# Performance work log

Measured on AMD Instinct MI355X. Metric: run time of the kernel, lower is better.

Reference implementation:

```python
import jax, jax.numpy as jnp
import numpy as np

N = 50000   # num nodes
E = 800000  # num edges
D = 128     # embedding dim
EPS = 1e-5


def setup_inputs() -> dict:
    key = jax.random.key(0)
    ks = jax.random.split(key, 16)
    x = jnp.arange(N, dtype=jnp.int32)
    edge_index = jax.random.randint(ks[0], (2, E), 0, N, dtype=jnp.int32)
    weight = jax.random.uniform(ks[1], (E,), dtype=jnp.float32)
    emb = jax.random.normal(ks[2], (N, D), dtype=jnp.float32)
    # layer dims: 128->128, 128->64, 64->32
    dims = [(128, 128), (128, 64), (64, 32)]
    inp = {"x": x, "edge_index": edge_index, "weight": weight, "emb": emb}
    for i, (fi, fo) in enumerate(dims, start=1):
        s = 1.0 / np.sqrt(fi)
        inp[f"W{i}"] = jax.random.uniform(ks[3 * i], (fi, fo), dtype=jnp.float32, minval=-s, maxval=s)
        inp[f"b{i}"] = jnp.zeros((fo,), dtype=jnp.float32)
        inp[f"g{i}"] = jnp.ones((fo,), dtype=jnp.float32)
        inp[f"be{i}"] = jnp.zeros((fo,), dtype=jnp.float32)
    return inp


def _gcn_conv(h, src, dst, w, W, b):
    # PyG GCNConv: linear, add self-loops (weight 1), symmetric normalization, scatter-add
    h = h @ W  # [N, Fout]
    loop = jnp.arange(N, dtype=src.dtype)
    src_l = jnp.concatenate([src, loop])
    dst_l = jnp.concatenate([dst, loop])
    w_l = jnp.concatenate([w, jnp.ones((N,), w.dtype)])
    deg = jax.ops.segment_sum(w_l, dst_l, num_segments=N)
    dinv = jnp.where(deg > 0, jax.lax.rsqrt(jnp.maximum(deg, 1e-30)), 0.0)
    norm = dinv[src_l] * w_l * dinv[dst_l]  # [E+N]
    msg = h[src_l] * norm[:, None]          # gather + scale, [E+N, Fout]
    out = jax.ops.segment_sum(msg, dst_l, num_segments=N)
    return out + b


def _batch_norm(h, g, be):
    mu = h.mean(axis=0)
    var = h.var(axis=0)  # biased, as torch BN uses for normalization
    return (h - mu) * jax.lax.rsqrt(var + EPS) * g + be


def reference(x, edge_index, weight, emb,
              W1, b1, g1, be1,
              W2, b2, g2, be2,
              W3, b3, g3, be3):
    src, dst = edge_index[0], edge_index[1]
    h = emb[x]  # embedding lookup
    h = _batch_norm(_gcn_conv(h, src, dst, weight, W1, b1), g1, be1)
    h = jax.nn.relu(h)
    h = _batch_norm(_gcn_conv(h, src, dst, weight, W2, b2), g2, be2)
    h = jax.nn.relu(h)
    h = _batch_norm(_gcn_conv(h, src, dst, weight, W3, b3), g3, be3)
    return h
```

## Files before the change

### kernel.cpp

```cpp
#include <hip/hip_runtime.h>
#include <hip/hip_bf16.h>

#define BN_EPS 1e-5f
#define FIXSCALE 16777216.0f
#define FIXINV   5.9604644775390625e-08
#define LOWMASK  0xFFFFFFFFFFULL

typedef __attribute__((ext_vector_type(8))) short bf16x8;
typedef __attribute__((ext_vector_type(4))) float f32x4;

__device__ __forceinline__ unsigned short bfu(float v) {
  return __bfloat16_as_ushort(__float2bfloat16(v));
}
__device__ __forceinline__ unsigned int pk_bf2(float a, float b) {
  return (unsigned int)bfu(a) | ((unsigned int)bfu(b) << 16);
}
__device__ __forceinline__ float bf_lo(unsigned int u) { return __uint_as_float(u << 16); }
__device__ __forceinline__ float bf_hi(unsigned int u) { return __uint_as_float(u & 0xFFFF0000u); }

__device__ __forceinline__ void fma8(float* a, uint4 u, float c) {
  a[0] += bf_lo(u.x) * c; a[1] += bf_hi(u.x) * c;
  a[2] += bf_lo(u.y) * c; a[3] += bf_hi(u.y) * c;
  a[4] += bf_lo(u.z) * c; a[5] += bf_hi(u.z) * c;
  a[6] += bf_lo(u.w) * c; a[7] += bf_hi(u.w) * c;
}

__device__ __forceinline__ float4 load4(const float* p) { return *(const float4*)p; }
__device__ __forceinline__ float4 load4(const unsigned short* p) {
  uint2 u = *(const uint2*)p;
  return make_float4(bf_lo(u.x), bf_hi(u.x), bf_lo(u.y), bf_hi(u.y));
}

template <int FIN, int FOUT>
constexpr int gemm_lds_bytes() {
  int stage = (64 * (FIN + 8) + FOUT * (FIN + 8)) * 2;
  int cb = 64 * (FOUT + 4) * 4;
  return stage > cb ? stage : cb;
}


__global__ void prep_k(const float* __restrict__ W1, const float* __restrict__ W2,
                       const float* __restrict__ W3, unsigned short* __restrict__ wt1,
                       unsigned short* __restrict__ wt2, unsigned short* __restrict__ wt3,
                       unsigned long long* __restrict__ packed, int n) {
  int idx = blockIdx.x * 256 + threadIdx.x;
  if (idx < n) packed[idx] = 0ULL;
  if (idx < 128 * 128) {
    int c = idx >> 7, k = idx & 127;
    wt1[idx] = bfu(W1[k * 128 + c]);
  } else if (idx < 128 * 128 + 128 * 64) {
    int i2 = idx - 128 * 128;
    int c = i2 >> 7, k = i2 & 127;
    wt2[i2] = bfu(W2[k * 64 + c]);
  } else if (idx < 128 * 128 + 128 * 64 + 64 * 32) {
    int i2 = idx - 128 * 128 - 128 * 64;
    int c = i2 >> 6, k = i2 & 63;
    wt3[i2] = bfu(W3[k * 32 + c]);
  }
}


__global__ __launch_bounds__(256) void hist_gemm1_k(
    const float* __restrict__ emb, const int* __restrict__ x,
    const unsigned short* __restrict__ wt1, unsigned short* __restrict__ outA,
    const int* __restrict__ dst, const float* __restrict__ w,
    unsigned long long* __restrict__ packed, int* __restrict__ rank,
    int n, int e, int gx) {
  constexpr int FIN = 128, FOUT = 128;
  constexpr int C4 = FIN / 4;
  constexpr int ldH = FIN + 8;
  constexpr int ldC = FOUT + 4;
  constexpr int NCT = FOUT / 16;
  constexpr int NK = FIN / 32;
  __shared__ __align__(16) char smem[64 * ldH * 2];
  unsigned short* Ht = (unsigned short*)smem;
  float* Cs = (float*)smem;

  if ((int)blockIdx.x >= gx) {
    int i = ((blockIdx.x - gx) * 256 + threadIdx.x) * 2;
    if (i + 1 < e) {
      int2 d2 = *(const int2*)(dst + i);
      float2 w2 = *(const float2*)(w + i);
      unsigned long long a0 = (1ULL << 40) | (unsigned long long)__float2uint_rn(w2.x * FIXSCALE);
      unsigned long long a1 = (1ULL << 40) | (unsigned long long)__float2uint_rn(w2.y * FIXSCALE);
      unsigned long long o0 = atomicAdd(&packed[d2.x], a0);
      unsigned long long o1 = atomicAdd(&packed[d2.y], a1);
      *(int2*)(rank + i) = make_int2((int)(o0 >> 40), (int)(o1 >> 40));
    } else if (i < e) {
      unsigned long long fw = (unsigned long long)__float2uint_rn(w[i] * FIXSCALE);
      unsigned long long old = atomicAdd(&packed[dst[i]], (1ULL << 40) | fw);
      rank[i] = (int)(old >> 40);
    }
    return;
  }

  const int t = threadIdx.x;
  const int r0 = blockIdx.x * 64;

  constexpr int NH = 64 * C4 / 256;
#pragma unroll
  for (int i = 0; i < NH; ++i) {
    int idx = t + 256 * i;
    int r = idx / C4, c4 = idx % C4;
    int gr = r0 + r;
    if (gr < n) {
      int srow = x[gr];
      float4 v = *(const float4*)(emb + (size_t)srow * FIN + c4 * 4);
      ushort4 p;
      p.x = bfu(v.x); p.y = bfu(v.y); p.z = bfu(v.z); p.w = bfu(v.w);
      *(ushort4*)&Ht[r * ldH + c4 * 4] = p;
    }
  }
  __syncthreads();

  const int wv = t >> 6;
  const int l = t & 63;
  const int l15 = l & 15;
  const int kg = l >> 4;
  const int arow = wv * 16 + l15;

  f32x4 acc[NCT];
#pragma unroll
  for (int c = 0; c < NCT; ++c) acc[c] = (f32x4){0.f, 0.f, 0.f, 0.f};

#pragma unroll
  for (int kk = 0; kk < NK; ++kk) {
    bf16x8 a = *(const bf16x8*)&Ht[arow * ldH + kk * 32 + kg * 8];
#pragma unroll
    for (int c = 0; c < NCT; ++c) {
      bf16x8 b = *(const bf16x8*)&wt1[(size_t)(c * 16 + l15) * FIN + kk * 32 + kg * 8];
      acc[c] = __builtin_amdgcn_mfma_f32_16x16x32_bf16(a, b, acc[c], 0, 0, 0);
    }
  }
  __syncthreads();

#pragma unroll
  for (int ph = 0; ph < 2; ++ph) {
    if ((wv >> 1) == ph) {
#pragma unroll
      for (int c = 0; c < NCT; ++c)
#pragma unroll
        for (int m = 0; m < 4; ++m)
          Cs[((wv & 1) * 16 + kg * 4 + m) * ldC + c * 16 + l15] = acc[c][m];
    }
    __syncthreads();
#pragma unroll
    for (int i = 0; i < 2; ++i) {
      int u = t + 256 * i;
      int r = u / (FOUT / 8), c8 = u % (FOUT / 8);
      int gr = r0 + ph * 32 + r;
      if (gr < n) {
        const float* p = &Cs[r * ldC + c8 * 8];
        float4 v0 = *(const float4*)p;
        float4 v1 = *(const float4*)(p + 4);
        uint4 o;
        o.x = pk_bf2(v0.x, v0.y); o.y = pk_bf2(v0.z, v0.w);
        o.z = pk_bf2(v1.x, v1.y); o.w = pk_bf2(v1.z, v1.w);
        *(uint4*)&outA[(size_t)gr * FOUT + c8 * 8] = o;
      }
    }
    if (ph == 0) __syncthreads();
  }
}


template <typename TIN, int FIN, int FOUT, bool BNIN>
__global__ __launch_bounds__(256) void gemm_mfma_k(
    const TIN* __restrict__ H, const float* __restrict__ scale, const float* __restrict__ shift,
    const unsigned short* __restrict__ WtG, unsigned short* __restrict__ out, int n) {
  constexpr int C4 = FIN / 4;
  constexpr int ldH = FIN + 8;
  constexpr int ldW = FIN + 8;
  constexpr int ldC = FOUT + 4;
  constexpr int NCT = FOUT / 16;
  constexpr int NK = FIN / 32;
  constexpr int HT_SH = 64 * ldH;

  __shared__ __align__(16) char smem[gemm_lds_bytes<FIN, FOUT>()];
  unsigned short* Ht = (unsigned short*)smem;
  unsigned short* Wt = (unsigned short*)smem + HT_SH;
  float* Cs = (float*)smem;

  const int t = threadIdx.x;
  const int r0 = blockIdx.x * 64;

  constexpr int NH = 64 * C4 / 256;
#pragma unroll
  for (int i = 0; i < NH; ++i) {
    int idx = t + 256 * i;
    int r = idx / C4, c4 = idx % C4;
    int gr = r0 + r;
    if (gr < n) {
      float4 v = load4(H + (size_t)gr * FIN + c4 * 4);
      if (BNIN) {
        float4 sc = *(const float4*)(scale + c4 * 4);
        float4 sh = *(const float4*)(shift + c4 * 4);
        v.x = fmaxf(v.x * sc.x + sh.x, 0.f);
        v.y = fmaxf(v.y * sc.y + sh.y, 0.f);
        v.z = fmaxf(v.z * sc.z + sh.z, 0.f);
        v.w = fmaxf(v.w * sc.w + sh.w, 0.f);
      }
      ushort4 p;
      p.x = bfu(v.x); p.y = bfu(v.y); p.z = bfu(v.z); p.w = bfu(v.w);
      *(ushort4*)&Ht[r * ldH + c4 * 4] = p;
    }
  }
  constexpr int NWU = FOUT * FIN / 8 / 256;
#pragma unroll
  for (int i = 0; i < NWU; ++i) {
    int idx = t + 256 * i;
    int wr = idx / (FIN / 8), w8 = idx % (FIN / 8);
    *(uint4*)&Wt[wr * ldW + w8 * 8] = *(const uint4*)&WtG[wr * FIN + w8 * 8];
  }
  __syncthreads();

  const int w = t >> 6;
  const int l = t & 63;
  const int l15 = l & 15;
  const int kg = l >> 4;
  const int arow = w * 16 + l15;

  f32x4 acc[NCT];
#pragma unroll
  for (int c = 0; c < NCT; ++c) acc[c] = (f32x4){0.f, 0.f, 0.f, 0.f};

#pragma unroll
  for (int kk = 0; kk < NK; ++kk) {
    bf16x8 a = *(const bf16x8*)&Ht[arow * ldH + kk * 32 + kg * 8];
#pragma unroll
    for (int c = 0; c < NCT; ++c) {
      bf16x8 b = *(const bf16x8*)&Wt[(c * 16 + l15) * ldW + kk * 32 + kg * 8];
      acc[c] = __builtin_amdgcn_mfma_f32_16x16x32_bf16(a, b, acc[c], 0, 0, 0);
    }
  }
  __syncthreads();

#pragma unroll
  for (int c = 0; c < NCT; ++c)
#pragma unroll
    for (int m = 0; m < 4; ++m)
      Cs[(w * 16 + kg * 4 + m) * ldC + c * 16 + l15] = acc[c][m];
  __syncthreads();

  constexpr int NU = 64 * FOUT / 8 / 256;
#pragma unroll
  for (int i = 0; i < NU; ++i) {
    int u = t + 256 * i;
    int r = u / (FOUT / 8), c8 = u % (FOUT / 8);
    int gr = r0 + r;
    if (gr < n) {
      const float* p = &Cs[r * ldC + c8 * 8];
      float4 v0 = *(const float4*)p;
      float4 v1 = *(const float4*)(p + 4);
      uint4 o;
      o.x = pk_bf2(v0.x, v0.y); o.y = pk_bf2(v0.z, v0.w);
      o.z = pk_bf2(v1.x, v1.y); o.w = pk_bf2(v1.z, v1.w);
      *(uint4*)&out[(size_t)gr * FOUT + c8 * 8] = o;
    }
  }
}


__global__ void scan_partial_k(const unsigned long long* __restrict__ packed,
                               int* __restrict__ bsum, float* __restrict__ dinv, int n) {
  __shared__ int s[256];
  int idx = blockIdx.x * 256 + threadIdx.x;
  unsigned long long p = (idx < n) ? packed[idx] : 0ULL;
  if (idx < n)
    dinv[idx] = rsqrtf(1.0f + (float)((double)(p & LOWMASK) * FIXINV));
  s[threadIdx.x] = (int)(p >> 40);
  __syncthreads();
  for (int off = 128; off > 0; off >>= 1) {
    if (threadIdx.x < off) s[threadIdx.x] += s[threadIdx.x + off];
    __syncthreads();
  }
  if (threadIdx.x == 0) bsum[blockIdx.x] = s[0];
}

__global__ void scan_final_k(const unsigned long long* __restrict__ packed,
                             const int* __restrict__ bsum, int* __restrict__ rowptr,
                             int n, int nb) {
  __shared__ int sb[256];
  __shared__ int s[256];
  const int b = blockIdx.x, t = threadIdx.x;

  int bv = (t < nb) ? bsum[t] : 0;
  sb[t] = bv;
  __syncthreads();
  for (int off = 1; off < 256; off <<= 1) {
    int u = (t >= off) ? sb[t - off] : 0;
    __syncthreads();
    sb[t] += u;
    __syncthreads();
  }
  const int blockbase = (b == 0) ? 0 : sb[b - 1];
  if (b == 0 && t == 0) rowptr[n] = sb[nb - 1];

  int idx = b * 256 + t;
  int v = (idx < n) ? (int)(packed[idx] >> 40) : 0;
  s[t] = v;
  __syncthreads();
  for (int off = 1; off < 256; off <<= 1) {
    int u = (t >= off) ? s[t - off] : 0;
    __syncthreads();
    s[t] += u;
    __syncthreads();
  }
  if (idx < n) rowptr[idx] = blockbase + s[t] - v;
}

__global__ void scatter_nb_k(const int* __restrict__ src, const int* __restrict__ dst,
                             const float* __restrict__ w, const int* __restrict__ rank,
                             const float* __restrict__ dinv, const int* __restrict__ rowptr,
                             int2* __restrict__ csr, int e) {
  int i = (blockIdx.x * blockDim.x + threadIdx.x) * 2;
  if (i + 1 < e) {
    int2 s2 = *(const int2*)(src + i);
    int2 d2 = *(const int2*)(dst + i);
    float2 w2 = *(const float2*)(w + i);
    int2 r2 = *(const int2*)(rank + i);
    int p0 = rowptr[d2.x] + r2.x;
    int p1 = rowptr[d2.y] + r2.y;
    csr[p0] = make_int2(s2.x, __float_as_int(dinv[s2.x] * w2.x * dinv[d2.x]));
    csr[p1] = make_int2(s2.y, __float_as_int(dinv[s2.y] * w2.y * dinv[d2.y]));
  } else if (i < e) {
    int d = dst[i], s = src[i];
    int pos = rowptr[d] + rank[i];
    csr[pos] = make_int2(s, __float_as_int(dinv[s] * w[i] * dinv[d]));
  }
}


template <int FOUT>
__global__ __launch_bounds__(256) void agg_csr_k(
    const unsigned short* __restrict__ hW, const int* __restrict__ rowptr,
    const int2* __restrict__ csr, const float* __restrict__ dinv,
    const float* __restrict__ b, unsigned short* __restrict__ out,
    float* __restrict__ psum, float* __restrict__ psq, int n) {
  constexpr int TPR = FOUT / 8;
  constexpr int RPB = 256 / TPR;
  const int t = threadIdx.x;
  const int j = t % TPR;
  const int rp = t / TPR;
  const int row = blockIdx.x * RPB + rp;
  const bool valid = row < n;

  float a[8] = {0.f, 0.f, 0.f, 0.f, 0.f, 0.f, 0.f, 0.f};
  if (valid) {
    const float di = dinv[row];
    const float c0 = di * di;
    {
      uint4 hu = *(const uint4*)(hW + (size_t)row * FOUT + j * 8);
      const float4 bb0 = *(const float4*)(b + j * 8);
      const float4 bb1 = *(const float4*)(b + j * 8 + 4);
      a[0] = bb0.x; a[1] = bb0.y; a[2] = bb0.z; a[3] = bb0.w;
      a[4] = bb1.x; a[5] = bb1.y; a[6] = bb1.z; a[7] = bb1.w;
      fma8(a, hu, c0);
    }
    const int e0 = rowptr[row], e1 = rowptr[row + 1];
    int ee = e0;
    for (; ee + 1 < e1; ee += 2) {
      const int2 d0 = csr[ee];
      const int2 d1 = csr[ee + 1];
      const uint4 u0 = *(const uint4*)(hW + (size_t)d0.x * FOUT + j * 8);
      const uint4 u1 = *(const uint4*)(hW + (size_t)d1.x * FOUT + j * 8);
      fma8(a, u0, __int_as_float(d0.y));
      fma8(a, u1, __int_as_float(d1.y));
    }
    if (ee < e1) {
      const int2 d0 = csr[ee];
      const uint4 u0 = *(const uint4*)(hW + (size_t)d0.x * FOUT + j * 8);
      fma8(a, u0, __int_as_float(d0.y));
    }
    uint4 o;
    o.x = pk_bf2(a[0], a[1]); o.y = pk_bf2(a[2], a[3]);
    o.z = pk_bf2(a[4], a[5]); o.w = pk_bf2(a[6], a[7]);
    *(uint4*)&out[(size_t)row * FOUT + j * 8] = o;
  }

  __shared__ float4 ls0[256], ls1[256], lq0[256], lq1[256];
  ls0[t] = make_float4(a[0], a[1], a[2], a[3]);
  ls1[t] = make_float4(a[4], a[5], a[6], a[7]);
  lq0[t] = make_float4(a[0] * a[0], a[1] * a[1], a[2] * a[2], a[3] * a[3]);
  lq1[t] = make_float4(a[4] * a[4], a[5] * a[5], a[6] * a[6], a[7] * a[7]);
  __syncthreads();
#pragma unroll
  for (int off = RPB / 2; off > 0; off >>= 1) {
    if (rp < off) {
      int o = off * TPR;
      float4 p, q;
      p = ls0[t]; q = ls0[t + o]; ls0[t] = make_float4(p.x + q.x, p.y + q.y, p.z + q.z, p.w + q.w);
      p = ls1[t]; q = ls1[t + o]; ls1[t] = make_float4(p.x + q.x, p.y + q.y, p.z + q.z, p.w + q.w);
      p = lq0[t]; q = lq0[t + o]; lq0[t] = make_float4(p.x + q.x, p.y + q.y, p.z + q.z, p.w + q.w);
      p = lq1[t]; q = lq1[t + o]; lq1[t] = make_float4(p.x + q.x, p.y + q.y, p.z + q.z, p.w + q.w);
    }
    __syncthreads();
  }
  if (rp == 0) {
    *(float4*)&psum[(size_t)blockIdx.x * FOUT + j * 8] = ls0[j];
    *(float4*)&psum[(size_t)blockIdx.x * FOUT + j * 8 + 4] = ls1[j];
    *(float4*)&psq[(size_t)blockIdx.x * FOUT + j * 8] = lq0[j];
    *(float4*)&psq[(size_t)blockIdx.x * FOUT + j * 8 + 4] = lq1[j];
  }
}


template <int FOUT>
__global__ __launch_bounds__(256) void bn_fin_col_k(
    const float* __restrict__ psum, const float* __restrict__ psq,
    const float* __restrict__ g, const float* __restrict__ be,
    float* __restrict__ scale, float* __restrict__ shift, int nblk, int n) {
  const int col = blockIdx.x;
  const int t = threadIdx.x;
  float s = 0.f, q = 0.f;
  for (int i = t; i < nblk; i += 256) {
    s += psum[(size_t)i * FOUT + col];
    q += psq[(size_t)i * FOUT + col];
  }
  __shared__ float ss[256], qq[256];
  ss[t] = s;
  qq[t] = q;
  __syncthreads();
  for (int off = 128; off > 0; off >>= 1) {
    if (t < off) { ss[t] += ss[t + off]; qq[t] += qq[t + off]; }
    __syncthreads();
  }
  if (t == 0) {
    float inv_n = 1.0f / (float)n;
    float mu = ss[0] * inv_n;
    float var = qq[0] * inv_n - mu * mu;
    float sc = g[col] * rsqrtf(var + BN_EPS);
    scale[col] = sc;
    shift[col] = be[col] - mu * sc;
  }
}

__global__ void bn_apply32_k(const unsigned short* __restrict__ in,
                             const float* __restrict__ scale, const float* __restrict__ shift,
                             float* __restrict__ out, int n) {
  int gid = blockIdx.x * blockDim.x + threadIdx.x;
  int row = gid >> 2, j = gid & 3;
  if (row >= n) return;
  uint4 u = *(const uint4*)(in + (size_t)row * 32 + j * 8);
  float v[8] = {bf_lo(u.x), bf_hi(u.x), bf_lo(u.y), bf_hi(u.y),
                bf_lo(u.z), bf_hi(u.z), bf_lo(u.w), bf_hi(u.w)};
  const float4 sc0 = *(const float4*)(scale + j * 8);
  const float4 sc1 = *(const float4*)(scale + j * 8 + 4);
  const float4 sh0 = *(const float4*)(shift + j * 8);
  const float4 sh1 = *(const float4*)(shift + j * 8 + 4);
  float4 o0 = make_float4(v[0] * sc0.x + sh0.x, v[1] * sc0.y + sh0.y,
                          v[2] * sc0.z + sh0.z, v[3] * sc0.w + sh0.w);
  float4 o1 = make_float4(v[4] * sc1.x + sh1.x, v[5] * sc1.y + sh1.y,
                          v[6] * sc1.z + sh1.z, v[7] * sc1.w + sh1.w);
  float* p = out + (size_t)row * 32 + j * 8;
  *(float4*)p = o0;
  *(float4*)(p + 4) = o1;
}


static inline size_t pad4(size_t v) { return (v + 3) & ~(size_t)3; }

extern "C" void kernel_launch(void* const* d_in, const int* in_sizes, int n_in,
                              void* d_out, int out_size, void* d_ws, size_t ws_size,
                              hipStream_t stream) {
  const int* x = (const int*)d_in[0];
  const int* ei = (const int*)d_in[1];
  const float* w = (const float*)d_in[2];
  const float* emb = (const float*)d_in[3];
  const float* W1 = (const float*)d_in[4];
  const float* b1 = (const float*)d_in[5];
  const float* g1 = (const float*)d_in[6];
  const float* be1 = (const float*)d_in[7];
  const float* W2 = (const float*)d_in[8];
  const float* b2 = (const float*)d_in[9];
  const float* g2 = (const float*)d_in[10];
  const float* be2 = (const float*)d_in[11];
  const float* W3 = (const float*)d_in[12];
  const float* b3 = (const float*)d_in[13];
  const float* g3 = (const float*)d_in[14];
  const float* be3 = (const float*)d_in[15];

  const int n = in_sizes[0];
  const int e = in_sizes[2];
  const int* src = ei;
  const int* dst = ei + e;

  float* ws = (float*)d_ws;
  size_t off = 0;
  unsigned short* bufA16 = (unsigned short*)(ws + off); off += pad4((size_t)n * 64);
  unsigned short* bufB16 = (unsigned short*)(ws + off); off += pad4((size_t)n * 64);
  unsigned long long* packed = (unsigned long long*)(ws + off); off += pad4((size_t)n * 2);
  float* dinv = ws + off; off += pad4(n);
  int* rowptr = (int*)(ws + off); off += pad4(n + 1);
  int* rank = (int*)(ws + off); off += pad4(e);
  int2* csr = (int2*)(ws + off); off += pad4((size_t)e * 2);
  unsigned short* wt1 = (unsigned short*)(ws + off); off += 128 * 128 / 2;
  unsigned short* wt2 = (unsigned short*)(ws + off); off += 128 * 64 / 2;
  unsigned short* wt3 = (unsigned short*)(ws + off); off += 64 * 32 / 2;
  float* psum = ws + off; off += 400384;
  float* psq = ws + off; off += 400384;
  float* scale = ws + off; off += 128;
  float* shift = ws + off; off += 128;
  int* bsum = (int*)(ws + off); off += 256;

  const int B = 256;
  dim3 blk(B);
  const int nb = (n + 255) / 256;
  const int e2 = (e + 1) / 2;
  const int gx = (n + 63) / 64;
  const int nblk1 = (n + 15) / 16;
  const int nblk2 = (n + 31) / 32;
  const int nblk3 = (n + 63) / 64;

  prep_k<<<(n + B - 1) / B, blk, 0, stream>>>(W1, W2, W3, wt1, wt2, wt3, packed, n);
  hist_gemm1_k<<<gx + (e2 + B - 1) / B, blk, 0, stream>>>(emb, x, wt1, bufA16, dst, w, packed, rank, n, e, gx);
  scan_partial_k<<<nb, blk, 0, stream>>>(packed, bsum, dinv, n);
  scan_final_k<<<nb, blk, 0, stream>>>(packed, bsum, rowptr, n, nb);
  scatter_nb_k<<<(e2 + B - 1) / B, blk, 0, stream>>>(src, dst, w, rank, dinv, rowptr, csr, e);

  agg_csr_k<128><<<nblk1, blk, 0, stream>>>(bufA16, rowptr, csr, dinv, b1, bufB16, psum, psq, n);
  bn_fin_col_k<128><<<128, blk, 0, stream>>>(psum, psq, g1, be1, scale, shift, nblk1, n);

  gemm_mfma_k<unsigned short, 128, 64, true><<<gx, blk, 0, stream>>>(bufB16, scale, shift, wt2, bufA16, n);
  agg_csr_k<64><<<nblk2, blk, 0, stream>>>(bufA16, rowptr, csr, dinv, b2, bufB16, psum, psq, n);
  bn_fin_col_k<64><<<64, blk, 0, stream>>>(psum, psq, g2, be2, scale, shift, nblk2, n);

  gemm_mfma_k<unsigned short, 64, 32, true><<<gx, blk, 0, stream>>>(bufB16, scale, shift, wt3, bufA16, n);
  agg_csr_k<32><<<nblk3, blk, 0, stream>>>(bufA16, rowptr, csr, dinv, b3, bufB16, psum, psq, n);
  bn_fin_col_k<32><<<32, blk, 0, stream>>>(psum, psq, g3, be3, scale, shift, nblk3, n);
  bn_apply32_k<<<((size_t)n * 4 + B - 1) / B, blk, 0, stream>>>(bufB16, scale, shift, (float*)d_out, n);
}
```

Measured before the change: 184.6 us.

## Use grid-stride loop in CSR aggregation with fixed grid and nontemporal edge loads

The aggregation kernel now launches a fixed grid of 1024 blocks and walks rows in a grid-stride loop. Each thread keeps running per-column sums and squared sums in registers, so the per-block partial BN statistics buffer shrinks and the column-finalize kernel reduces over far fewer partials. CSR edge records are read with nontemporal loads to keep them out of the cache hierarchy. The fixed grid may leave less parallelism to hide the latency of the irregular gathers, since each block handles several rows in sequence.

```diff
diff --git a/kernel.cpp b/kernel.cpp
--- a/kernel.cpp
+++ b/kernel.cpp
@@ -342,17 +342,21 @@
   const int t = threadIdx.x;
   const int j = t % TPR;
   const int rp = t / TPR;
-  const int row = blockIdx.x * RPB + rp;
-  const bool valid = row < n;
-
-  float a[8] = {0.f, 0.f, 0.f, 0.f, 0.f, 0.f, 0.f, 0.f};
-  if (valid) {
+
+  float sreg[8] = {0.f, 0.f, 0.f, 0.f, 0.f, 0.f, 0.f, 0.f};
+  float qreg[8] = {0.f, 0.f, 0.f, 0.f, 0.f, 0.f, 0.f, 0.f};
+
+  const float4 bb0 = *(const float4*)(b + j * 8);
+  const float4 bb1 = *(const float4*)(b + j * 8 + 4);
+
+  for (int base = blockIdx.x * RPB; base < n; base += gridDim.x * RPB) {
+    const int row = base + rp;
+    if (row >= n) continue;
+    float a[8];
     const float di = dinv[row];
     const float c0 = di * di;
     {
       uint4 hu = *(const uint4*)(hW + (size_t)row * FOUT + j * 8);
-      const float4 bb0 = *(const float4*)(b + j * 8);
-      const float4 bb1 = *(const float4*)(b + j * 8 + 4);
       a[0] = bb0.x; a[1] = bb0.y; a[2] = bb0.z; a[3] = bb0.w;
       a[4] = bb1.x; a[5] = bb1.y; a[6] = bb1.z; a[7] = bb1.w;
       fma8(a, hu, c0);
@@ -360,29 +364,37 @@
     const int e0 = rowptr[row], e1 = rowptr[row + 1];
     int ee = e0;
     for (; ee + 1 < e1; ee += 2) {
-      const int2 d0 = csr[ee];
-      const int2 d1 = csr[ee + 1];
-      const uint4 u0 = *(const uint4*)(hW + (size_t)d0.x * FOUT + j * 8);
-      const uint4 u1 = *(const uint4*)(hW + (size_t)d1.x * FOUT + j * 8);
-      fma8(a, u0, __int_as_float(d0.y));
-      fma8(a, u1, __int_as_float(d1.y));
+      long long ev0 = __builtin_nontemporal_load((const long long*)(csr + ee));
+      long long ev1 = __builtin_nontemporal_load((const long long*)(csr + ee + 1));
+      int s0 = (int)(unsigned int)ev0;
+      int s1 = (int)(unsigned int)ev1;
+      float c0e = __int_as_float((int)(ev0 >> 32));
+      float c1e = __int_as_float((int)(ev1 >> 32));
+      const uint4 u0 = *(const uint4*)(hW + (size_t)s0 * FOUT + j * 8);
+      const uint4 u1 = *(const uint4*)(hW + (size_t)s1 * FOUT + j * 8);
+      fma8(a, u0, c0e);
+      fma8(a, u1, c1e);
     }
     if (ee < e1) {
-      const int2 d0 = csr[ee];
-      const uint4 u0 = *(const uint4*)(hW + (size_t)d0.x * FOUT + j * 8);
-      fma8(a, u0, __int_as_float(d0.y));
+      long long ev0 = __builtin_nontemporal_load((const long long*)(csr + ee));
+      int s0 = (int)(unsigned int)ev0;
+      float c0e = __int_as_float((int)(ev0 >> 32));
+      const uint4 u0 = *(const uint4*)(hW + (size_t)s0 * FOUT + j * 8);
+      fma8(a, u0, c0e);
     }
     uint4 o;
     o.x = pk_bf2(a[0], a[1]); o.y = pk_bf2(a[2], a[3]);
     o.z = pk_bf2(a[4], a[5]); o.w = pk_bf2(a[6], a[7]);
     *(uint4*)&out[(size_t)row * FOUT + j * 8] = o;
+#pragma unroll
+    for (int k = 0; k < 8; ++k) { sreg[k] += a[k]; qreg[k] += a[k] * a[k]; }
   }
 
   __shared__ float4 ls0[256], ls1[256], lq0[256], lq1[256];
-  ls0[t] = make_float4(a[0], a[1], a[2], a[3]);
-  ls1[t] = make_float4(a[4], a[5], a[6], a[7]);
-  lq0[t] = make_float4(a[0] * a[0], a[1] * a[1], a[2] * a[2], a[3] * a[3]);
-  lq1[t] = make_float4(a[4] * a[4], a[5] * a[5], a[6] * a[6], a[7] * a[7]);
+  ls0[t] = make_float4(sreg[0], sreg[1], sreg[2], sreg[3]);
+  ls1[t] = make_float4(sreg[4], sreg[5], sreg[6], sreg[7]);
+  lq0[t] = make_float4(qreg[0], qreg[1], qreg[2], qreg[3]);
+  lq1[t] = make_float4(qreg[4], qreg[5], qreg[6], qreg[7]);
   __syncthreads();
 #pragma unroll
   for (int off = RPB / 2; off > 0; off >>= 1) {
@@ -497,8 +509,8 @@
   unsigned short* wt1 = (unsigned short*)(ws + off); off += 128 * 128 / 2;
   unsigned short* wt2 = (unsigned short*)(ws + off); off += 128 * 64 / 2;
   unsigned short* wt3 = (unsigned short*)(ws + off); off += 64 * 32 / 2;
-  float* psum = ws + off; off += 400384;
-  float* psq = ws + off; off += 400384;
+  float* psum = ws + off; off += 131072;
+  float* psq = ws + off; off += 131072;
   float* scale = ws + off; off += 128;
   float* shift = ws + off; off += 128;
   int* bsum = (int*)(ws + off); off += 256;
@@ -508,9 +520,7 @@
   const int nb = (n + 255) / 256;
   const int e2 = (e + 1) / 2;
   const int gx = (n + 63) / 64;
-  const int nblk1 = (n + 15) / 16;
-  const int nblk2 = (n + 31) / 32;
-  const int nblk3 = (n + 63) / 64;
+  const int AG = 1024;
 
   prep_k<<<(n + B - 1) / B, blk, 0, stream>>>(W1, W2, W3, wt1, wt2, wt3, packed, n);
   hist_gemm1_k<<<gx + (e2 + B - 1) / B, blk, 0, stream>>>(emb, x, wt1, bufA16, dst, w, packed, rank, n, e, gx);
@@ -518,15 +528,15 @@
   scan_final_k<<<nb, blk, 0, stream>>>(packed, bsum, rowptr, n, nb);
   scatter_nb_k<<<(e2 + B - 1) / B, blk, 0, stream>>>(src, dst, w, rank, dinv, rowptr, csr, e);
 
-  agg_csr_k<128><<<nblk1, blk, 0, stream>>>(bufA16, rowptr, csr, dinv, b1, bufB16, psum, psq, n);
-  bn_fin_col_k<128><<<128, blk, 0, stream>>>(psum, psq, g1, be1, scale, shift, nblk1, n);
+  agg_csr_k<128><<<AG, blk, 0, stream>>>(bufA16, rowptr, csr, dinv, b1, bufB16, psum, psq, n);
+  bn_fin_col_k<128><<<128, blk, 0, stream>>>(psum, psq, g1, be1, scale, shift, AG, n);
 
   gemm_mfma_k<unsigned short, 128, 64, true><<<gx, blk, 0, stream>>>(bufB16, scale, shift, wt2, bufA16, n);
-  agg_csr_k<64><<<nblk2, blk, 0, stream>>>(bufA16, rowptr, csr, dinv, b2, bufB16, psum, psq, n);
-  bn_fin_col_k<64><<<64, blk, 0, stream>>>(psum, psq, g2, be2, scale, shift, nblk2, n);
+  agg_csr_k<64><<<AG, blk, 0, stream>>>(bufA16, rowptr, csr, dinv, b2, bufB16, psum, psq, n);
+  bn_fin_col_k<64><<<64, blk, 0, stream>>>(psum, psq, g2, be2, scale, shift, AG, n);
 
   gemm_mfma_k<unsigned short, 64, 32, true><<<gx, blk, 0, stream>>>(bufB16, scale, shift, wt3, bufA16, n);
-  agg_csr_k<32><<<nblk3, blk, 0, stream>>>(bufA16, rowptr, csr, dinv, b3, bufB16, psum, psq, n);
-  bn_fin_col_k<32><<<32, blk, 0, stream>>>(psum, psq, g3, be3, scale, shift, nblk3, n);
+  agg_csr_k<32><<<AG, blk, 0, stream>>>(bufA16, rowptr, csr, dinv, b3, bufB16, psum, psq, n);
+  bn_fin_col_k<32><<<32, blk, 0, stream>>>(psum, psq, g3, be3, scale, shift, AG, n);
   bn_apply32_k<<<((size_t)n * 4 + B - 1) / B, blk, 0, stream>>>(bufB16, scale, shift, (float*)d_out, n);
 }
```

Result: slower. 209.5 us (+13.5%).
